# Performance work log

Measured on AMD Instinct MI355X. Metric: run time of the kernel, lower is better.

The kernel has to match this reference:

```python
import jax, jax.numpy as jnp
import numpy as np

B, T, C_EMB, C_HEAD = 4, 4096, 1024, 64

def setup_inputs() -> dict:
    key = jax.random.key(0)
    kx, kk, kq, kv = jax.random.split(key, 4)
    x = jax.random.normal(kx, (B, T, C_EMB), dtype=jnp.float32)
    # nn.Linear(C_EMB, C_HEAD, bias=False); store as (in, out) so projection is x @ W
    Wk = jax.random.normal(kk, (C_EMB, C_HEAD), dtype=jnp.float32) * 0.02
    Wq = jax.random.normal(kq, (C_EMB, C_HEAD), dtype=jnp.float32) * 0.02
    Wv = jax.random.normal(kv, (C_EMB, C_HEAD), dtype=jnp.float32) * 0.02
    return {"x": x, "Wk": Wk, "Wq": Wq, "Wv": Wv}

def reference(x, Wk, Wq, Wv):
    k = x @ Wk  # [B,T,Ch]
    q = x @ Wq
    v = x @ Wv
    scale = C_HEAD ** -0.5
    weights = jnp.einsum('bqc,bkc->bqk', q, k) * scale  # [B,T,T]
    causal = jnp.tril(jnp.ones((T, T), dtype=bool))
    weights = jnp.where(causal, weights, -jnp.inf)
    # NOTE: original uses F.softmax(dim=1), i.e. over the QUERY (row) axis -> axis=-2
    weights = jax.nn.softmax(weights, axis=-2)
    # dropout_rate=0.0 (eval) -> identity
    return jnp.einsum('bqk,bkc->bqc', weights, v)
```

## Files before the change

### kernel.cpp

```cpp
#include <hip/hip_runtime.h>
#include <math.h>

#define BB 4
#define TT 4096
#define CE 1024
#define CH 64
#define SCALE2 0.18033688011112042f
#define NQT 64
#define NZC 8
#define NZP 4

typedef unsigned short ushort_t;
typedef __attribute__((ext_vector_type(8))) short bf16x8;
typedef __attribute__((ext_vector_type(8))) unsigned short u16x8;
typedef __attribute__((ext_vector_type(4))) float f32x4;

__device__ __forceinline__ unsigned short f2bf(float f) {
    unsigned int x = __builtin_bit_cast(unsigned int, f);
    unsigned int r = x + 0x7fffu + ((x >> 16) & 1u);
    return (unsigned short)(r >> 16);
}
__device__ __forceinline__ float bf2f(unsigned short u) {
    unsigned int x = ((unsigned int)u) << 16;
    return __builtin_bit_cast(float, x);
}
__device__ __forceinline__ unsigned cvt_pk_bf16(float lo, float hi) {
    unsigned r;
    asm("v_cvt_pk_bf16_f32 %0, %1, %2" : "=v"(r) : "v"(lo), "v"(hi));
    return r;
}

__device__ __forceinline__ void stage_tile(const ushort_t* __restrict__ src,
                                           ushort_t (*dst)[68], int tg)
{
#pragma unroll
    for (int i = 0; i < 2; ++i) {
        const int idx = i * 256 + tg;
        const int row = idx >> 3, c0 = (idx & 7) * 8;
        u16x8 v = *(const u16x8*)(src + (long)idx * 8);
        union { u16x8 v; uint2 q[2]; } uu; uu.v = v;
        *(uint2*)&dst[row][c0]     = uu.q[0];
        *(uint2*)&dst[row][c0 + 4] = uu.q[1];
    }
}

__device__ __forceinline__ void stage_tile512(const ushort_t* __restrict__ src,
                                              ushort_t (*dst)[68], int tid)
{
    const int row = tid >> 3, c0 = (tid & 7) * 8;
    u16x8 v = *(const u16x8*)(src + (long)tid * 8);
    union { u16x8 v; uint2 q[2]; } uu; uu.v = v;
    *(uint2*)&dst[row][c0]     = uu.q[0];
    *(uint2*)&dst[row][c0 + 4] = uu.q[1];
}

__device__ __forceinline__ bf16x8 frag68(const ushort_t* p) {
    union { bf16x8 v; uint2 q[2]; } uu;
    uu.q[0] = *(const uint2*)p;
    uu.q[1] = *(const uint2*)(p + 4);
    return uu.v;
}

__global__ __launch_bounds__(256)
void wt_build(const float* __restrict__ Wk, const float* __restrict__ Wq,
              const float* __restrict__ Wv, ushort_t* __restrict__ wt2)
{
    const int m = blockIdx.x, kt = blockIdx.y;
    const float* __restrict__ W = (m == 0) ? Wk : (m == 1 ? Wq : Wv);
    const int k0 = kt * 64;
    __shared__ float lds[64][65];
    const int cc = threadIdx.x & 63, g = threadIdx.x >> 6;
#pragma unroll
    for (int i = 0; i < 16; ++i) {
        const int r = g * 16 + i;
        lds[r][cc] = W[(k0 + r) * CH + cc];
    }
    __syncthreads();
    const int k = k0 + cc;
#pragma unroll
    for (int i = 0; i < 16; ++i) {
        const int c = g * 16 + i;
        wt2[((long)(k >> 5) * 192 + (m * 64 + c)) * 32 + (k & 31)] = f2bf(lds[cc][c]);
    }
}

__global__ __launch_bounds__(512)
void proj_mfma(const float* __restrict__ x, const ushort_t* __restrict__ wt2,
               ushort_t* __restrict__ qb, ushort_t* __restrict__ kb, ushort_t* __restrict__ vb)
{
    const int tid = threadIdx.x;
    const int w = tid >> 6, l = tid & 63, lg = l >> 4, lr = l & 15;
    const int wr = w >> 2, wc = w & 3;
    const long t0 = (long)blockIdx.x * 32;

    __shared__ ushort_t As[2][32][68];
    __shared__ ushort_t Bs[2][192][68];

    f32x4 acc[3];
#pragma unroll
    for (int nf = 0; nf < 3; ++nf) acc[nf] = (f32x4){0.f, 0.f, 0.f, 0.f};

    const int arow = tid >> 4, acol = (tid & 15) * 4;
    const float* __restrict__ xsrc = x + (t0 + arow) * CE + acol;

    int bc[3], bh[3], bk[3];
#pragma unroll
    for (int i = 0; i < 3; ++i) {
        const int idx = i * 512 + tid;
        const int h = idx >= 768;
        const int j = idx - h * 768;
        bc[i] = j >> 2; bh[i] = h; bk[i] = (j & 3) * 8;
    }

    float4 a4 = *(const float4*)(xsrc);
    u16x8 bv[3];
#pragma unroll
    for (int i = 0; i < 3; ++i)
        bv[i] = *(const u16x8*)(wt2 + ((long)(bh[i]) * 192 + bc[i]) * 32 + bk[i]);
    {
        uint2 pk;
        pk.x = cvt_pk_bf16(a4.x, a4.y);
        pk.y = cvt_pk_bf16(a4.z, a4.w);
        *(uint2*)&As[0][arow][acol] = pk;
#pragma unroll
        for (int i = 0; i < 3; ++i) {
            union { u16x8 v; uint2 q[2]; } uu; uu.v = bv[i];
            ushort_t* d = &Bs[0][bc[i]][bh[i] * 32 + bk[i]];
            *(uint2*)d = uu.q[0];
            *(uint2*)(d + 4) = uu.q[1];
        }
    }
    a4 = *(const float4*)(xsrc + 64);
#pragma unroll
    for (int i = 0; i < 3; ++i)
        bv[i] = *(const u16x8*)(wt2 + ((long)(2 + bh[i]) * 192 + bc[i]) * 32 + bk[i]);
    __syncthreads();

    for (int step = 0; step < 16; ++step) {
        const int cur = step & 1;
        if (step + 1 < 16) {
            uint2 pk;
            pk.x = cvt_pk_bf16(a4.x, a4.y);
            pk.y = cvt_pk_bf16(a4.z, a4.w);
            *(uint2*)&As[cur ^ 1][arow][acol] = pk;
#pragma unroll
            for (int i = 0; i < 3; ++i) {
                union { u16x8 v; uint2 q[2]; } uu; uu.v = bv[i];
                ushort_t* d = &Bs[cur ^ 1][bc[i]][bh[i] * 32 + bk[i]];
                *(uint2*)d = uu.q[0];
                *(uint2*)(d + 4) = uu.q[1];
            }
        }
        if (step + 2 < 16) {
            a4 = *(const float4*)(xsrc + (step + 2) * 64);
            const int ktn = (step + 2) * 2;
#pragma unroll
            for (int i = 0; i < 3; ++i)
                bv[i] = *(const u16x8*)(wt2 + ((long)(ktn + bh[i]) * 192 + bc[i]) * 32 + bk[i]);
        }
#pragma unroll
        for (int h = 0; h < 2; ++h) {
            bf16x8 af = frag68(&As[cur][wr * 16 + lr][h * 32 + lg * 8]);
#pragma unroll
            for (int nf = 0; nf < 3; ++nf) {
                bf16x8 bf = frag68(&Bs[cur][wc * 48 + nf * 16 + lr][h * 32 + lg * 8]);
                acc[nf] = __builtin_amdgcn_mfma_f32_16x16x32_bf16(af, bf, acc[nf], 0, 0, 0);
            }
        }
        __syncthreads();
    }

    ushort_t* Os = &Bs[0][0][0];
#pragma unroll
    for (int nf = 0; nf < 3; ++nf)
#pragma unroll
        for (int r = 0; r < 4; ++r)
            Os[(wr * 16 + lg * 4 + r) * 200 + wc * 48 + nf * 16 + lr] = f2bf(acc[nf][r]);
    __syncthreads();
    if (tid < 256) {
        const int row = tid >> 3, c0 = (tid & 7) * 8;
#pragma unroll
        for (int m = 0; m < 3; ++m) {
            u16x8 ov = *(const u16x8*)&Os[row * 200 + m * 64 + c0];
            ushort_t* __restrict__ outp = (m == 0) ? kb : (m == 1 ? qb : vb);
            *(u16x8*)(outp + (t0 + row) * CH + c0) = ov;
        }
    }
}

__global__ __launch_bounds__(512)
void colstats_mfma(const ushort_t* __restrict__ qb, const ushort_t* __restrict__ kb,
                   float* __restrict__ pl)
{
    const int b = blockIdx.x, p = blockIdx.y, z = blockIdx.z;
    const int tid = threadIdx.x;
    const int w = tid >> 6, l = tid & 63, lg = l >> 4, lr = l & 15;
    const int wg = w >> 2, wc = w & 3, tg = tid & 255;
    const long baseT = (long)b * TT;
    const long NTT = (long)BB * TT;

    __shared__ ushort_t Ks[64][68], Qs[2][64][68];
    __shared__ float redc[4][64][5];

    for (int pass = 0; pass < 2; ++pass) {
        const int kt = pass ? (63 - p) : p;
        stage_tile512(kb + (baseT + (long)kt * 64) * CH, Ks, tid);
        __syncthreads();
        bf16x8 ka0 = frag68(&Ks[wc * 16 + lr][lg * 8]);
        bf16x8 ka1 = frag68(&Ks[wc * 16 + lr][32 + lg * 8]);

        float l_r[4] = {0.f, 0.f, 0.f, 0.f};

        const int j0 = kt + ((z - kt) & (NZC - 1));
        const int n0 = (j0 < NQT) ? ((NQT - 1 - j0) >> 4) + 1 : 0;
        for (int i = 0; i < n0; ++i) {
            const int j = j0 + NZC * wg + 2 * NZC * i;
            const bool act = (j < NQT);
            if (act) stage_tile(qb + (baseT + (long)j * 64) * CH, Qs[wg], tg);
            __syncthreads();
            if (act) {
                const bool diag = (j == kt);
#pragma unroll
                for (int qf = 0; qf < 4; ++qf) {
                    bf16x8 b0 = frag68(&Qs[wg][qf * 16 + lr][lg * 8]);
                    bf16x8 b1 = frag68(&Qs[wg][qf * 16 + lr][32 + lg * 8]);
                    f32x4 s = {0.f, 0.f, 0.f, 0.f};
                    s = __builtin_amdgcn_mfma_f32_16x16x32_bf16(ka0, b0, s, 0, 0, 0);
                    s = __builtin_amdgcn_mfma_f32_16x16x32_bf16(ka1, b1, s, 0, 0, 0);
#pragma unroll
                    for (int r = 0; r < 4; ++r) {
                        float ev = exp2f(s[r] * SCALE2);
                        if (diag && (qf * 16 + lr) < (wc * 16 + lg * 4 + r)) ev = 0.f;
                        l_r[r] += ev;
                    }
                }
            }
            __syncthreads();
        }
        if (wg == 1) {
#pragma unroll
            for (int r = 0; r < 4; ++r) redc[wc][l][r] = l_r[r];
        }
        __syncthreads();
        if (wg == 0) {
#pragma unroll
            for (int r = 0; r < 4; ++r) {
                float lv = l_r[r] + redc[wc][l][r];
                for (int d = 1; d < 16; d <<= 1) lv += __shfl_xor(lv, d);
                if (lr == 0) {
                    const long k = (long)kt * 64 + wc * 16 + lg * 4 + r;
                    pl[(long)z * NTT + baseT + k] = lv;
                }
            }
        }
        __syncthreads();
    }
}

__global__ __launch_bounds__(256)
void vt_scale(const ushort_t* __restrict__ vb, const float* __restrict__ pl,
              ushort_t* __restrict__ vtb2)
{
    const int b = blockIdx.x;
    const int jt = blockIdx.y;
    const long t0 = (long)jt * 64;
    const int tid = threadIdx.x;
    __shared__ ushort_t lds[64][72];
    const long baseT = (long)b * TT;
    const long NTT = (long)BB * TT;
#pragma unroll
    for (int i = 0; i < 2; ++i) {
        const int t = i * 32 + (tid >> 3);
        const int c0 = (tid & 7) * 8;
        u16x8 v = *(const u16x8*)(vb + (baseT + t0 + t) * CH + c0);
        const long idx = baseT + t0 + t;
        float ls = pl[idx];
#pragma unroll
        for (int zz = 1; zz < NZC; ++zz) ls += pl[zz * NTT + idx];
        const float sc = 1.f / ls;
#pragma unroll
        for (int j = 0; j < 8; ++j) lds[c0 + j][t] = f2bf(bf2f(v[j]) * sc);
    }
    __syncthreads();
    ushort_t* __restrict__ dst = vtb2 + ((long)(b * 64 + jt)) * (64 * 64);
#pragma unroll
    for (int i = 0; i < 2; ++i) {
        const int c = i * 32 + (tid >> 3);
        const int tt0 = (tid & 7) * 8;
        u16x8 ov = *(const u16x8*)&lds[c][tt0];
        *(u16x8*)(dst + (long)c * 64 + tt0) = ov;
    }
}

__global__ __launch_bounds__(512)
void pv_mfma(const ushort_t* __restrict__ qb, const ushort_t* __restrict__ kb,
             const ushort_t* __restrict__ vtb2, ushort_t* __restrict__ pout)
{
    const int b = blockIdx.x, p = blockIdx.y, z = blockIdx.z;
    const int tid = threadIdx.x;
    const int w = tid >> 6, l = tid & 63, lg = l >> 4, lr = l & 15;
    const int wg = w >> 2, wc = w & 3, tg = tid & 255;
    const long baseT = (long)b * TT;
    const long NTT = (long)BB * TT;

    __shared__ ushort_t Qs[64][68], Ks[2][64][68], Vs[2][64][68], Ps[2][64][68];
    __shared__ float redp[4][64][17];

    for (int pass = 0; pass < 2; ++pass) {
        const int qt = pass ? (63 - p) : p;
        stage_tile512(qb + (baseT + (long)qt * 64) * CH, Qs, tid);
        __syncthreads();
        bf16x8 qf_[4][2];
#pragma unroll
        for (int qf = 0; qf < 4; ++qf) {
            qf_[qf][0] = frag68(&Qs[qf * 16 + lr][lg * 8]);
            qf_[qf][1] = frag68(&Qs[qf * 16 + lr][32 + lg * 8]);
        }
        f32x4 o[4];
#pragma unroll
        for (int qf = 0; qf < 4; ++qf) o[qf] = (f32x4){0.f, 0.f, 0.f, 0.f};

        const int n0 = (qt >= z) ? ((qt - z) >> 3) + 1 : 0;
        for (int i = 0; i < n0; ++i) {
            const int j = z + 4 * wg + 8 * i;
            const bool act = (j <= qt);
            if (act) {
                stage_tile(kb + (baseT + (long)j * 64) * CH, Ks[wg], tg);
                stage_tile(vtb2 + ((long)(b * 64 + j)) * (64 * 64), Vs[wg], tg);
            }
            __syncthreads();
            bf16x8 va0, va1;
            if (act) {
                bf16x8 ka0 = frag68(&Ks[wg][wc * 16 + lr][lg * 8]);
                bf16x8 ka1 = frag68(&Ks[wg][wc * 16 + lr][32 + lg * 8]);
                va0 = frag68(&Vs[wg][wc * 16 + lr][lg * 8]);
                va1 = frag68(&Vs[wg][wc * 16 + lr][32 + lg * 8]);
                const bool diag = (j == qt);
#pragma unroll
                for (int qf = 0; qf < 4; ++qf) {
                    f32x4 s = {0.f, 0.f, 0.f, 0.f};
                    s = __builtin_amdgcn_mfma_f32_16x16x32_bf16(ka0, qf_[qf][0], s, 0, 0, 0);
                    s = __builtin_amdgcn_mfma_f32_16x16x32_bf16(ka1, qf_[qf][1], s, 0, 0, 0);
                    float ev[4];
#pragma unroll
                    for (int r = 0; r < 4; ++r) {
                        ev[r] = exp2f(s[r] * SCALE2);
                        if (diag && (qf * 16 + lr) < (wc * 16 + lg * 4 + r)) ev[r] = 0.f;
                    }
                    uint2 pk;
                    pk.x = cvt_pk_bf16(ev[0], ev[1]);
                    pk.y = cvt_pk_bf16(ev[2], ev[3]);
                    *(uint2*)&Ps[wg][qf * 16 + lr][wc * 16 + lg * 4] = pk;
                }
            }
            __syncthreads();
            if (act) {
#pragma unroll
                for (int qf = 0; qf < 4; ++qf) {
                    bf16x8 p0 = frag68(&Ps[wg][qf * 16 + lr][lg * 8]);
                    bf16x8 p1 = frag68(&Ps[wg][qf * 16 + lr][32 + lg * 8]);
                    o[qf] = __builtin_amdgcn_mfma_f32_16x16x32_bf16(va0, p0, o[qf], 0, 0, 0);
                    o[qf] = __builtin_amdgcn_mfma_f32_16x16x32_bf16(va1, p1, o[qf], 0, 0, 0);
                }
            }
        }
        if (wg == 1) {
#pragma unroll
            for (int qf = 0; qf < 4; ++qf)
#pragma unroll
                for (int r = 0; r < 4; ++r) redp[wc][l][qf * 4 + r] = o[qf][r];
        }
        __syncthreads();
        if (wg == 0) {
            ushort_t* pz = pout + ((long)z * NTT + baseT + (long)qt * 64) * CH;
#pragma unroll
            for (int qf = 0; qf < 4; ++qf) {
                f32x4 ov = o[qf];
#pragma unroll
                for (int r = 0; r < 4; ++r) ov[r] += redp[wc][l][qf * 4 + r];
                uint2 pk;
                pk.x = cvt_pk_bf16(ov[0], ov[1]);
                pk.y = cvt_pk_bf16(ov[2], ov[3]);
                *(uint2*)(pz + (long)(qf * 16 + lr) * CH + wc * 16 + lg * 4) = pk;
            }
        }
        __syncthreads();
    }
}

__global__ __launch_bounds__(256)
void finalize_out(const ushort_t* __restrict__ pout, float* __restrict__ out)
{
    const long i = (long)blockIdx.x * 256 + threadIdx.x;
    const long ne = (long)BB * TT * CH;
    float s0 = 0.f, s1 = 0.f, s2 = 0.f, s3 = 0.f;
#pragma unroll
    for (int zz = 0; zz < NZP; ++zz) {
        uint2 a = *(const uint2*)(pout + zz * ne + i * 4);
        s0 += bf2f((unsigned short)(a.x & 0xffffu));
        s1 += bf2f((unsigned short)(a.x >> 16));
        s2 += bf2f((unsigned short)(a.y & 0xffffu));
        s3 += bf2f((unsigned short)(a.y >> 16));
    }
    float4 r; r.x = s0; r.y = s1; r.z = s2; r.w = s3;
    reinterpret_cast<float4*>(out)[i] = r;
}

extern "C" void kernel_launch(void* const* d_in, const int* in_sizes, int n_in,
                              void* d_out, int out_size, void* d_ws, size_t ws_size,
                              hipStream_t stream)
{
    const float* x  = (const float*)d_in[0];
    const float* Wk = (const float*)d_in[1];
    const float* Wq = (const float*)d_in[2];
    const float* Wv = (const float*)d_in[3];
    float* out = (float*)d_out;

    const size_t NT = (size_t)BB * TT;
    ushort_t* qb   = (ushort_t*)d_ws;
    ushort_t* kb   = qb + NT * CH;
    ushort_t* vb   = kb + NT * CH;
    ushort_t* vtb2 = vb + NT * CH;
    ushort_t* wt2  = vtb2 + NT * CH;
    float* pl      = (float*)(wt2 + 192 * CE);
    ushort_t* pout = (ushort_t*)(pl + NZC * NT);

    hipLaunchKernelGGL(wt_build, dim3(3, 16), dim3(256), 0, stream,
                       Wk, Wq, Wv, wt2);
    hipLaunchKernelGGL(proj_mfma, dim3(NT / 32), dim3(512), 0, stream,
                       x, wt2, qb, kb, vb);
    hipLaunchKernelGGL(colstats_mfma, dim3(BB, NQT / 2, NZC), dim3(512), 0, stream,
                       qb, kb, pl);
    hipLaunchKernelGGL(vt_scale, dim3(BB, TT / 64), dim3(256), 0, stream,
                       vb, pl, vtb2);
    hipLaunchKernelGGL(pv_mfma, dim3(BB, NQT / 2, NZP), dim3(512), 0, stream,
                       qb, kb, vtb2, pout);
    hipLaunchKernelGGL(finalize_out, dim3(NT * CH / 4 / 256), dim3(256), 0, stream,
                       pout, out);
}
```

Measured before the change: 71.92 us.

## Use single-buffered 128-wide K tiles in projection GEMM, halving loop steps

```diff
diff --git a/kernel.cpp b/kernel.cpp
--- a/kernel.cpp
+++ b/kernel.cpp
@@ -93,8 +93,8 @@
     const int wr = w >> 2, wc = w & 3;
     const long t0 = (long)blockIdx.x * 32;
 
-    __shared__ ushort_t As[2][32][68];
-    __shared__ ushort_t Bs[2][192][68];
+    __shared__ ushort_t As[32][132];
+    __shared__ ushort_t Bs[192][132];
 
     f32x4 acc[3];
 #pragma unroll
@@ -103,74 +103,62 @@
     const int arow = tid >> 4, acol = (tid & 15) * 4;
     const float* __restrict__ xsrc = x + (t0 + arow) * CE + acol;
 
-    int bc[3], bh[3], bk[3];
-#pragma unroll
-    for (int i = 0; i < 3; ++i) {
+    int bc[6], bh[6], bk[6];
+#pragma unroll
+    for (int i = 0; i < 6; ++i) {
         const int idx = i * 512 + tid;
-        const int h = idx >= 768;
+        const int h = idx / 768;
         const int j = idx - h * 768;
         bc[i] = j >> 2; bh[i] = h; bk[i] = (j & 3) * 8;
     }
 
-    float4 a4 = *(const float4*)(xsrc);
-    u16x8 bv[3];
-#pragma unroll
-    for (int i = 0; i < 3; ++i)
+    float4 a4[2];
+    u16x8 bv[6];
+    a4[0] = *(const float4*)(xsrc);
+    a4[1] = *(const float4*)(xsrc + 64);
+#pragma unroll
+    for (int i = 0; i < 6; ++i)
         bv[i] = *(const u16x8*)(wt2 + ((long)(bh[i]) * 192 + bc[i]) * 32 + bk[i]);
-    {
-        uint2 pk;
-        pk.x = cvt_pk_bf16(a4.x, a4.y);
-        pk.y = cvt_pk_bf16(a4.z, a4.w);
-        *(uint2*)&As[0][arow][acol] = pk;
-#pragma unroll
-        for (int i = 0; i < 3; ++i) {
-            union { u16x8 v; uint2 q[2]; } uu; uu.v = bv[i];
-            ushort_t* d = &Bs[0][bc[i]][bh[i] * 32 + bk[i]];
-            *(uint2*)d = uu.q[0];
-            *(uint2*)(d + 4) = uu.q[1];
-        }
-    }
-    a4 = *(const float4*)(xsrc + 64);
-#pragma unroll
-    for (int i = 0; i < 3; ++i)
-        bv[i] = *(const u16x8*)(wt2 + ((long)(2 + bh[i]) * 192 + bc[i]) * 32 + bk[i]);
-    __syncthreads();
-
-    for (int step = 0; step < 16; ++step) {
-        const int cur = step & 1;
-        if (step + 1 < 16) {
-            uint2 pk;
-            pk.x = cvt_pk_bf16(a4.x, a4.y);
-            pk.y = cvt_pk_bf16(a4.z, a4.w);
-            *(uint2*)&As[cur ^ 1][arow][acol] = pk;
-#pragma unroll
-            for (int i = 0; i < 3; ++i) {
+
+    for (int step = 0; step < 8; ++step) {
+        {
+            uint2 pk0, pk1;
+            pk0.x = cvt_pk_bf16(a4[0].x, a4[0].y);
+            pk0.y = cvt_pk_bf16(a4[0].z, a4[0].w);
+            pk1.x = cvt_pk_bf16(a4[1].x, a4[1].y);
+            pk1.y = cvt_pk_bf16(a4[1].z, a4[1].w);
+            *(uint2*)&As[arow][acol]      = pk0;
+            *(uint2*)&As[arow][acol + 64] = pk1;
+#pragma unroll
+            for (int i = 0; i < 6; ++i) {
                 union { u16x8 v; uint2 q[2]; } uu; uu.v = bv[i];
-                ushort_t* d = &Bs[cur ^ 1][bc[i]][bh[i] * 32 + bk[i]];
+                ushort_t* d = &Bs[bc[i]][bh[i] * 32 + bk[i]];
                 *(uint2*)d = uu.q[0];
                 *(uint2*)(d + 4) = uu.q[1];
             }
         }
-        if (step + 2 < 16) {
-            a4 = *(const float4*)(xsrc + (step + 2) * 64);
-            const int ktn = (step + 2) * 2;
-#pragma unroll
-            for (int i = 0; i < 3; ++i)
+        __syncthreads();
+        if (step + 1 < 8) {
+            a4[0] = *(const float4*)(xsrc + (step + 1) * 128);
+            a4[1] = *(const float4*)(xsrc + (step + 1) * 128 + 64);
+            const int ktn = (step + 1) * 4;
+#pragma unroll
+            for (int i = 0; i < 6; ++i)
                 bv[i] = *(const u16x8*)(wt2 + ((long)(ktn + bh[i]) * 192 + bc[i]) * 32 + bk[i]);
         }
 #pragma unroll
-        for (int h = 0; h < 2; ++h) {
-            bf16x8 af = frag68(&As[cur][wr * 16 + lr][h * 32 + lg * 8]);
+        for (int h = 0; h < 4; ++h) {
+            bf16x8 af = frag68(&As[wr * 16 + lr][h * 32 + lg * 8]);
 #pragma unroll
             for (int nf = 0; nf < 3; ++nf) {
-                bf16x8 bf = frag68(&Bs[cur][wc * 48 + nf * 16 + lr][h * 32 + lg * 8]);
+                bf16x8 bf = frag68(&Bs[wc * 48 + nf * 16 + lr][h * 32 + lg * 8]);
                 acc[nf] = __builtin_amdgcn_mfma_f32_16x16x32_bf16(af, bf, acc[nf], 0, 0, 0);
             }
         }
         __syncthreads();
     }
 
-    ushort_t* Os = &Bs[0][0][0];
+    ushort_t* Os = &Bs[0][0];
 #pragma unroll
     for (int nf = 0; nf < 3; ++nf)
 #pragma unroll
```

Result: slower. 73.73 us (+2.5%).
